# Kernel optimization log

Measured on AMD Instinct MI355X. Metric: run time of the kernel, lower is better.

Reference implementation:

```python
import jax, jax.numpy as jnp
import numpy as np


def setup_inputs() -> dict:
    key = jax.random.key(0)
    k1, k2 = jax.random.split(key)
    B, Tc, Tq, D = 8, 2048, 1024, 1024
    similarity = jax.random.normal(k1, (B, Tc, Tq), dtype=jnp.float32)
    qencode = jax.random.normal(k2, (B, Tq, D), dtype=jnp.float32)
    return {"similarity": similarity, "qencode": qencode}


def reference(similarity, qencode):
    # softmax over query axis, then weighted sum of query encodings:
    # equivalent to softmax(similarity, -1) @ qencode, avoiding the
    # [B, Tc, Tq, D] broadcasted intermediate of the original TF code.
    attn = jax.nn.softmax(similarity, axis=-1)          # [B, Tc, Tq]
    c2q = jnp.einsum("bcq,bqd->bcd", attn, qencode)     # [B, Tc, D]
    return c2q
```

## Files before the change

### kernel.cpp

```cpp
#include <hip/hip_runtime.h>
#include <hip/hip_bf16.h>
#include <stdint.h>

#define BATCH 8
#define TC 2048
#define TQ 1024
#define DD 1024

typedef __attribute__((ext_vector_type(8))) __bf16 bf16x8;
typedef __attribute__((ext_vector_type(4))) float f32x4;

__device__ __forceinline__ ushort f2bf(float f) {
    uint32_t u = __float_as_uint(f);
    uint32_t r = (u + 0x7fffu + ((u >> 16) & 1u)) >> 16;
    return (ushort)r;
}

__global__ __launch_bounds__(256) void softmax_rows(const float* __restrict__ sim,
                                                    ushort* __restrict__ attn) {
    const int wid = threadIdx.x >> 6;
    const int lane = threadIdx.x & 63;
    const int row = blockIdx.x * 4 + wid;
    const float4* src = (const float4*)(sim + (size_t)row * TQ);

    float4 x[4];
    #pragma unroll
    for (int j = 0; j < 4; j++) x[j] = src[lane + 64 * j];

    float m = -INFINITY;
    #pragma unroll
    for (int j = 0; j < 4; j++)
        m = fmaxf(m, fmaxf(fmaxf(x[j].x, x[j].y), fmaxf(x[j].z, x[j].w)));
    #pragma unroll
    for (int o = 32; o >= 1; o >>= 1) m = fmaxf(m, __shfl_xor(m, o));

    const float L2E = 1.4426950408889634f;
    float e[4][4];
    float s = 0.f;
    #pragma unroll
    for (int j = 0; j < 4; j++) {
        e[j][0] = exp2f((x[j].x - m) * L2E);
        e[j][1] = exp2f((x[j].y - m) * L2E);
        e[j][2] = exp2f((x[j].z - m) * L2E);
        e[j][3] = exp2f((x[j].w - m) * L2E);
        s += (e[j][0] + e[j][1]) + (e[j][2] + e[j][3]);
    }
    #pragma unroll
    for (int o = 32; o >= 1; o >>= 1) s += __shfl_xor(s, o);
    const float inv = 1.0f / s;

    ushort4* dst = (ushort4*)(attn + (size_t)row * TQ);
    #pragma unroll
    for (int j = 0; j < 4; j++) {
        ushort4 o4;
        o4.x = f2bf(e[j][0] * inv);
        o4.y = f2bf(e[j][1] * inv);
        o4.z = f2bf(e[j][2] * inv);
        o4.w = f2bf(e[j][3] * inv);
        dst[lane + 64 * j] = o4;
    }
}

__global__ __launch_bounds__(256) void transpose_cast(const float* __restrict__ q,
                                                      ushort* __restrict__ qt) {
    __shared__ float tile[64][65];
    const int b = blockIdx.z;
    const int q0 = blockIdx.y * 64;
    const int d0 = blockIdx.x * 64;
    const int t = threadIdx.x;
    const int r = t >> 4;
    const int c = (t & 15) * 4;

    #pragma unroll
    for (int it = 0; it < 4; it++) {
        float4 v = *(const float4*)(q + ((size_t)b * TQ + q0 + r + it * 16) * DD + d0 + c);
        tile[r + it * 16][c + 0] = v.x;
        tile[r + it * 16][c + 1] = v.y;
        tile[r + it * 16][c + 2] = v.z;
        tile[r + it * 16][c + 3] = v.w;
    }
    __syncthreads();

    #pragma unroll
    for (int it = 0; it < 4; it++) {
        const int d = (t >> 4) + it * 16;
        const int qq = (t & 15) * 4;
        ushort4 o4;
        o4.x = f2bf(tile[qq + 0][d]);
        o4.y = f2bf(tile[qq + 1][d]);
        o4.z = f2bf(tile[qq + 2][d]);
        o4.w = f2bf(tile[qq + 3][d]);
        *(ushort4*)(qt + ((size_t)b * DD + d0 + d) * TQ + q0 + qq) = o4;
    }
}

__global__ __launch_bounds__(256, 2) void gemm_bf16(const ushort* __restrict__ A,
                                                    const ushort* __restrict__ Bt,
                                                    float* __restrict__ C) {
    __shared__ __align__(16) ushort As[128 * 32];
    __shared__ __align__(16) ushort Bs[128 * 32];

    const int flat = blockIdx.x;
    const int b = flat >> 7;
    const int rem = flat & 127;
    const int group = rem >> 5;
    const int mi_t = group * 4 + (rem & 3);
    const int ni_t = (rem >> 2) & 7;
    const int tm0 = mi_t * 128;
    const int tn0 = ni_t * 128;

    const ushort* Ab = A + (size_t)b * TC * TQ;
    const ushort* Bb = Bt + (size_t)b * DD * TQ;
    float* Cb = C + (size_t)b * TC * DD;

    const int t = threadIdx.x;
    const int w = t >> 6, lane = t & 63;
    const int quad = lane >> 4, l16 = lane & 15;
    const int wm = (w >> 1) * 64, wn = (w & 1) * 64;

    f32x4 acc[4][4];
    #pragma unroll
    for (int i = 0; i < 4; i++)
        #pragma unroll
        for (int j = 0; j < 4; j++) acc[i][j] = (f32x4){0.f, 0.f, 0.f, 0.f};

    const int srow = w * 16 + (lane >> 2);
    const int sk = (lane & 3) * 8;

    for (int kk = 0; kk < TQ; kk += 32) {
        #pragma unroll
        for (int j = 0; j < 2; j++) {
            const ushort* ga = Ab + (size_t)(tm0 + j * 64 + srow) * TQ + kk + sk;
            const ushort* gb = Bb + (size_t)(tn0 + j * 64 + srow) * TQ + kk + sk;
            char* la = (char*)As + j * 4096 + w * 1024;
            char* lb = (char*)Bs + j * 4096 + w * 1024;
            __builtin_amdgcn_global_load_lds(
                (const __attribute__((address_space(1))) void*)ga,
                (__attribute__((address_space(3))) void*)la, 16, 0, 0);
            __builtin_amdgcn_global_load_lds(
                (const __attribute__((address_space(1))) void*)gb,
                (__attribute__((address_space(3))) void*)lb, 16, 0, 0);
        }
        __syncthreads();

        bf16x8 af[4], bfr[4];
        #pragma unroll
        for (int mi = 0; mi < 4; mi++)
            af[mi] = *(const bf16x8*)&As[(wm + mi * 16 + l16) * 32 + quad * 8];
        #pragma unroll
        for (int ni = 0; ni < 4; ni++)
            bfr[ni] = *(const bf16x8*)&Bs[(wn + ni * 16 + l16) * 32 + quad * 8];

        #pragma unroll
        for (int mi = 0; mi < 4; mi++)
            #pragma unroll
            for (int ni = 0; ni < 4; ni++)
                acc[mi][ni] = __builtin_amdgcn_mfma_f32_16x16x32_bf16(
                    af[mi], bfr[ni], acc[mi][ni], 0, 0, 0);
        __syncthreads();
    }

    #pragma unroll
    for (int mi = 0; mi < 4; mi++) {
        const int r0 = tm0 + wm + mi * 16 + quad * 4;
        #pragma unroll
        for (int ni = 0; ni < 4; ni++) {
            const int c = tn0 + wn + ni * 16 + l16;
            f32x4 v = acc[mi][ni];
            #pragma unroll
            for (int r = 0; r < 4; r++) Cb[(size_t)(r0 + r) * DD + c] = v[r];
        }
    }
}

extern "C" void kernel_launch(void* const* d_in, const int* in_sizes, int n_in,
                              void* d_out, int out_size, void* d_ws, size_t ws_size,
                              hipStream_t stream) {
    const float* sim = (const float*)d_in[0];
    const float* qen = (const float*)d_in[1];
    float* out = (float*)d_out;

    ushort* attn = (ushort*)d_ws;
    ushort* qt = (ushort*)d_ws + (size_t)BATCH * TC * TQ;

    softmax_rows<<<BATCH * TC / 4, 256, 0, stream>>>(sim, attn);
    transpose_cast<<<dim3(DD / 64, TQ / 64, BATCH), 256, 0, stream>>>(qen, qt);
    gemm_bf16<<<BATCH * (TC / 128) * (DD / 128), 256, 0, stream>>>(attn, qt, out);
}
```

Measured before the change: 186.2 us.

## Merge softmax and transpose into one prep launch; XOR-swizzle GEMM LDS tiles

Combines the softmax and transpose-cast kernels into a single launch that dispatches by block index, removing one kernel launch and letting the two independent passes overlap. In the GEMM, the global-to-LDS load column and the fragment read column are XOR-swizzled by row bits, meant to reduce LDS bank conflicts on the bf16x8 reads. The swizzle must match between the writer and reader mappings. The merged kernel also reserves shared memory for every block, including softmax blocks that never use it, which could lower occupancy for those blocks.

```diff
diff --git a/kernel.cpp b/kernel.cpp
--- a/kernel.cpp
+++ b/kernel.cpp
@@ -16,81 +16,84 @@
     return (ushort)r;
 }
 
-__global__ __launch_bounds__(256) void softmax_rows(const float* __restrict__ sim,
-                                                    ushort* __restrict__ attn) {
-    const int wid = threadIdx.x >> 6;
-    const int lane = threadIdx.x & 63;
-    const int row = blockIdx.x * 4 + wid;
-    const float4* src = (const float4*)(sim + (size_t)row * TQ);
+__global__ __launch_bounds__(256) void prep(const float* __restrict__ sim,
+                                            const float* __restrict__ qen,
+                                            ushort* __restrict__ attn,
+                                            ushort* __restrict__ qt) {
+    __shared__ float tile[64][65];
+    const int t = threadIdx.x;
+    if (blockIdx.x < 4096) {
+        const int wid = t >> 6;
+        const int lane = t & 63;
+        const int row = blockIdx.x * 4 + wid;
+        const float4* src = (const float4*)(sim + (size_t)row * TQ);
 
-    float4 x[4];
-    #pragma unroll
-    for (int j = 0; j < 4; j++) x[j] = src[lane + 64 * j];
+        float4 x[4];
+        #pragma unroll
+        for (int j = 0; j < 4; j++) x[j] = src[lane + 64 * j];
 
-    float m = -INFINITY;
-    #pragma unroll
-    for (int j = 0; j < 4; j++)
-        m = fmaxf(m, fmaxf(fmaxf(x[j].x, x[j].y), fmaxf(x[j].z, x[j].w)));
-    #pragma unroll
-    for (int o = 32; o >= 1; o >>= 1) m = fmaxf(m, __shfl_xor(m, o));
+        float m = -INFINITY;
+        #pragma unroll
+        for (int j = 0; j < 4; j++)
+            m = fmaxf(m, fmaxf(fmaxf(x[j].x, x[j].y), fmaxf(x[j].z, x[j].w)));
+        #pragma unroll
+        for (int o = 32; o >= 1; o >>= 1) m = fmaxf(m, __shfl_xor(m, o));
 
-    const float L2E = 1.4426950408889634f;
-    float e[4][4];
-    float s = 0.f;
-    #pragma unroll
-    for (int j = 0; j < 4; j++) {
-        e[j][0] = exp2f((x[j].x - m) * L2E);
-        e[j][1] = exp2f((x[j].y - m) * L2E);
-        e[j][2] = exp2f((x[j].z - m) * L2E);
-        e[j][3] = exp2f((x[j].w - m) * L2E);
-        s += (e[j][0] + e[j][1]) + (e[j][2] + e[j][3]);
-    }
-    #pragma unroll
-    for (int o = 32; o >= 1; o >>= 1) s += __shfl_xor(s, o);
-    const float inv = 1.0f / s;
+        const float L2E = 1.4426950408889634f;
+        float e[4][4];
+        float s = 0.f;
+        #pragma unroll
+        for (int j = 0; j < 4; j++) {
+            e[j][0] = exp2f((x[j].x - m) * L2E);
+            e[j][1] = exp2f((x[j].y - m) * L2E);
+            e[j][2] = exp2f((x[j].z - m) * L2E);
+            e[j][3] = exp2f((x[j].w - m) * L2E);
+            s += (e[j][0] + e[j][1]) + (e[j][2] + e[j][3]);
+        }
+        #pragma unroll
+        for (int o = 32; o >= 1; o >>= 1) s += __shfl_xor(s, o);
+        const float inv = 1.0f / s;
 
-    ushort4* dst = (ushort4*)(attn + (size_t)row * TQ);
-    #pragma unroll
-    for (int j = 0; j < 4; j++) {
-        ushort4 o4;
-        o4.x = f2bf(e[j][0] * inv);
-        o4.y = f2bf(e[j][1] * inv);
-        o4.z = f2bf(e[j][2] * inv);
-        o4.w = f2bf(e[j][3] * inv);
-        dst[lane + 64 * j] = o4;
-    }
-}
+        ushort4* dst = (ushort4*)(attn + (size_t)row * TQ);
+        #pragma unroll
+        for (int j = 0; j < 4; j++) {
+            ushort4 o4;
+            o4.x = f2bf(e[j][0] * inv);
+            o4.y = f2bf(e[j][1] * inv);
+            o4.z = f2bf(e[j][2] * inv);
+            o4.w = f2bf(e[j][3] * inv);
+            dst[lane + 64 * j] = o4;
+        }
+    } else {
+        const int bid = blockIdx.x - 4096;
+        const int b = bid >> 8;
+        const int rem = bid & 255;
+        const int q0 = (rem >> 4) * 64;
+        const int d0 = (rem & 15) * 64;
+        const int r = t >> 4;
+        const int c = (t & 15) * 4;
 
-__global__ __launch_bounds__(256) void transpose_cast(const float* __restrict__ q,
-                                                      ushort* __restrict__ qt) {
-    __shared__ float tile[64][65];
-    const int b = blockIdx.z;
-    const int q0 = blockIdx.y * 64;
-    const int d0 = blockIdx.x * 64;
-    const int t = threadIdx.x;
-    const int r = t >> 4;
-    const int c = (t & 15) * 4;
+        #pragma unroll
+        for (int it = 0; it < 4; it++) {
+            float4 v = *(const float4*)(qen + ((size_t)b * TQ + q0 + r + it * 16) * DD + d0 + c);
+            tile[r + it * 16][c + 0] = v.x;
+            tile[r + it * 16][c + 1] = v.y;
+            tile[r + it * 16][c + 2] = v.z;
+            tile[r + it * 16][c + 3] = v.w;
+        }
+        __syncthreads();
 
-    #pragma unroll
-    for (int it = 0; it < 4; it++) {
-        float4 v = *(const float4*)(q + ((size_t)b * TQ + q0 + r + it * 16) * DD + d0 + c);
-        tile[r + it * 16][c + 0] = v.x;
-        tile[r + it * 16][c + 1] = v.y;
-        tile[r + it * 16][c + 2] = v.z;
-        tile[r + it * 16][c + 3] = v.w;
-    }
-    __syncthreads();
-
-    #pragma unroll
-    for (int it = 0; it < 4; it++) {
-        const int d = (t >> 4) + it * 16;
-        const int qq = (t & 15) * 4;
-        ushort4 o4;
-        o4.x = f2bf(tile[qq + 0][d]);
-        o4.y = f2bf(tile[qq + 1][d]);
-        o4.z = f2bf(tile[qq + 2][d]);
-        o4.w = f2bf(tile[qq + 3][d]);
-        *(ushort4*)(qt + ((size_t)b * DD + d0 + d) * TQ + q0 + qq) = o4;
+        #pragma unroll
+        for (int it = 0; it < 4; it++) {
+            const int d = (t >> 4) + it * 16;
+            const int qq = (t & 15) * 4;
+            ushort4 o4;
+            o4.x = f2bf(tile[qq + 0][d]);
+            o4.y = f2bf(tile[qq + 1][d]);
+            o4.z = f2bf(tile[qq + 2][d]);
+            o4.w = f2bf(tile[qq + 3][d]);
+            *(ushort4*)(qt + ((size_t)b * DD + d0 + d) * TQ + q0 + qq) = o4;
+        }
     }
 }
 
@@ -125,7 +128,9 @@
         for (int j = 0; j < 4; j++) acc[i][j] = (f32x4){0.f, 0.f, 0.f, 0.f};
 
     const int srow = w * 16 + (lane >> 2);
-    const int sk = (lane & 3) * 8;
+    const int sk = ((lane & 3) ^ ((lane >> 3) & 3)) * 8;
+
+    const int rswz = (quad ^ ((l16 >> 1) & 3)) * 8;
 
     for (int kk = 0; kk < TQ; kk += 32) {
         #pragma unroll
@@ -146,10 +151,10 @@
         bf16x8 af[4], bfr[4];
         #pragma unroll
         for (int mi = 0; mi < 4; mi++)
-            af[mi] = *(const bf16x8*)&As[(wm + mi * 16 + l16) * 32 + quad * 8];
+            af[mi] = *(const bf16x8*)&As[(wm + mi * 16 + l16) * 32 + rswz];
         #pragma unroll
         for (int ni = 0; ni < 4; ni++)
-            bfr[ni] = *(const bf16x8*)&Bs[(wn + ni * 16 + l16) * 32 + quad * 8];
+            bfr[ni] = *(const bf16x8*)&Bs[(wn + ni * 16 + l16) * 32 + rswz];
 
         #pragma unroll
         for (int mi = 0; mi < 4; mi++)
@@ -183,7 +188,6 @@
     ushort* attn = (ushort*)d_ws;
     ushort* qt = (ushort*)d_ws + (size_t)BATCH * TC * TQ;
 
-    softmax_rows<<<BATCH * TC / 4, 256, 0, stream>>>(sim, attn);
-    transpose_cast<<<dim3(DD / 64, TQ / 64, BATCH), 256, 0, stream>>>(qen, qt);
+    prep<<<4096 + 2048, 256, 0, stream>>>(sim, qen, attn, qt);
     gemm_bf16<<<BATCH * (TC / 128) * (DD / 128), 256, 0, stream>>>(attn, qt, out);
 }
```

Result: no change. 184.1 us (-1.1%).
